# Optimization experiments

Hardware: AMD Instinct MI355X
Metric: run time of the kernel (lower is better)

The kernel has to match this reference:

```python
import jax, jax.numpy as jnp
import numpy as np

N = 50000      # nodes
E = 400000     # edges
HID = 128      # hidden_size
L = 3          # num_att_layer
K = 9          # rbf_size
H = 4          # heads
C = HID // H   # out_channels per head (32)
G = 512        # graphs in batch
CUTOFF = 10.0


def _rbf(D):
    # ExponentialRBF: softplus(softplus_inverse(x)) == x, so centers/widths are the raw values
    centers = jnp.linspace(1.0, float(np.exp(-CUTOFF)), K)          # (K,)
    width = (0.5 / ((1.0 - np.exp(-CUTOFF)) / K)) ** 2              # scalar
    x = D / CUTOFF
    x3 = x ** 3
    x4 = x3 * x
    x5 = x4 * x
    cut = jnp.where(x < 1.0, 1.0 - 6.0 * x5 + 15.0 * x4 - 10.0 * x3, 0.0)
    return cut[:, None] * jnp.exp(-width * (jnp.exp(-D)[:, None] - centers) ** 2)  # (E,K)


def _ln(x, g, b):
    mu = jnp.mean(x, axis=-1, keepdims=True)
    var = jnp.var(x, axis=-1, keepdims=True)
    return (x - mu) / jnp.sqrt(var + 1e-5) * g + b


def _seg_softmax(logits, seg, n):
    # numerically stable softmax over edges grouped by target node
    m = jax.ops.segment_max(logits, seg, num_segments=n)
    e = jnp.exp(logits - m[seg])
    s = jax.ops.segment_sum(e, seg, num_segments=n)
    return e / s[seg]


def setup_inputs() -> dict:
    key = jax.random.key(0)
    ks = jax.random.split(key, 32)
    s = 1.0 / np.sqrt(HID)
    se = 1.0 / np.sqrt(K + 1)
    sb = 1.0 / np.sqrt(3 * HID)
    nrm = jax.random.normal
    inp = {
        "h": nrm(ks[0], (N, HID), jnp.float32),
        "pos": nrm(ks[1], (N, 3), jnp.float32) * 3.0,
        "edge_weight": jax.random.uniform(ks[2], (E,), jnp.float32),
        "Wq": nrm(ks[3], (L, HID, HID)) * s,   "bq": nrm(ks[4], (L, HID)) * 0.01,
        "Wk": nrm(ks[5], (L, HID, HID)) * s,   "bk": nrm(ks[6], (L, HID)) * 0.01,
        "Wv": nrm(ks[7], (L, HID, HID)) * s,   "bv": nrm(ks[8], (L, HID)) * 0.01,
        "We": nrm(ks[9], (L, K + 1, HID)) * se,
        "Wskip": nrm(ks[10], (L, HID, HID)) * s, "bskip": nrm(ks[11], (L, HID)) * 0.01,
        "Wbeta": nrm(ks[12], (L, 3 * HID, 1)) * sb,
        "Wffn1": nrm(ks[13], (L, HID, HID)) * s, "bffn1": nrm(ks[14], (L, HID)) * 0.01,
        "Wffn2": nrm(ks[15], (L, HID, HID)) * s, "bffn2": nrm(ks[16], (L, HID)) * 0.01,
        "Wffn3": nrm(ks[17], (L, HID, HID)) * s, "bffn3": nrm(ks[18], (L, HID)) * 0.01,
        "ln_g": jnp.ones((HID,), jnp.float32),
        "ln_b": jnp.zeros((HID,), jnp.float32),
        "Wo1": nrm(ks[19], (HID, HID)) * s, "bo1": nrm(ks[20], (HID,)) * 0.01,
        "Wo2": nrm(ks[21], (HID, 1)) * s,   "bo2": nrm(ks[22], (1,)) * 0.01,
        "edge_index": jax.random.randint(ks[23], (2, E), 0, N),
        "batch": jnp.sort(jax.random.randint(ks[24], (N,), 0, G)),
    }
    return inp


def reference(h, pos, edge_weight, Wq, bq, Wk, bk, Wv, bv, We, Wskip, bskip, Wbeta,
              Wffn1, bffn1, Wffn2, bffn2, Wffn3, bffn3, ln_g, ln_b, Wo1, bo1, Wo2, bo2,
              edge_index, batch):
    sp = jax.nn.softplus
    n = h.shape[0]
    src, dst = edge_index[0], edge_index[1]  # source j -> target i
    D = jnp.linalg.norm(pos[dst] - pos[src], axis=-1)              # (E,)
    efeat = jnp.concatenate([_rbf(D), edge_weight[:, None]], -1)   # (E, K+1)
    inv_sqrt_c = 1.0 / np.sqrt(C)

    for i in range(L):
        hn = _ln(h, ln_g, ln_b)
        q = (hn @ Wq[i] + bq[i]).reshape(n, H, C)
        k = (hn @ Wk[i] + bk[i]).reshape(n, H, C)
        v = (hn @ Wv[i] + bv[i]).reshape(n, H, C)
        ea = (efeat @ We[i]).reshape(-1, H, C)                     # (E,H,C)
        kj = k[src] + ea
        alpha = jnp.einsum('ehc,ehc->eh', q[dst], kj) * inv_sqrt_c  # (E,H)
        alpha = _seg_softmax(alpha, dst, n)
        # dropout p=0.5 is a no-op in eval mode
        msg = (v[src] + ea) * alpha[:, :, None]
        out = jax.ops.segment_sum(msg, dst, num_segments=n).reshape(n, H * C)
        x_r = hn @ Wskip[i] + bskip[i]
        beta = jax.nn.sigmoid(jnp.concatenate([out, x_r, out - x_r], -1) @ Wbeta[i])
        out = beta * x_r + (1.0 - beta) * out
        h = hn + sp(out)
        hn2 = _ln(h, ln_g, ln_b)
        f = sp(hn2 @ Wffn1[i] + bffn1[i])
        f = sp(f @ Wffn2[i] + bffn2[i])
        f = sp(f @ Wffn3[i] + bffn3[i])
        h = hn2 + f

    pooled = jax.ops.segment_sum(h, batch, num_segments=G)          # (G, HID)
    return sp(pooled @ Wo1 + bo1) @ Wo2 + bo2                       # (G, 1)
```

## Files before the change

### kernel.cpp

```cpp
#include <hip/hip_runtime.h>
#include <hip/hip_bf16.h>
#include <math.h>

#define HID 128
#define KRBF 9
#define NLAYER 3
#define QSSTR 320
#define KVSTR 256
#define QWCOLS 576

typedef __attribute__((ext_vector_type(8))) short bf16x8;
typedef __attribute__((ext_vector_type(4))) float f32x4;

__device__ __forceinline__ float sp_(float x){ return fmaxf(x,0.f) + log1pf(expf(-fabsf(x))); }
__device__ __forceinline__ float sigm_(float x){ return 1.f/(1.f+expf(-x)); }
__device__ __forceinline__ float b2f(short s){
  union{unsigned u; float f;} x; x.u = ((unsigned)(unsigned short)s)<<16; return x.f;
}
__device__ __forceinline__ float wsum64(float v){
  #pragma unroll
  for(int m=1;m<64;m<<=1) v += __shfl_xor(v,m,64);
  return v;
}
__device__ __forceinline__ float wsum16(float v){
  #pragma unroll
  for(int m=1;m<16;m<<=1) v += __shfl_xor(v,m,64);
  return v;
}
__device__ __forceinline__ float2 ldbf2(const __hip_bfloat16* p){
  __hip_bfloat162 b = *(const __hip_bfloat162*)p;
  return make_float2(__bfloat162float(b.x), __bfloat162float(b.y));
}
__device__ __forceinline__ int lb_(const int* __restrict__ a, int n, int key){
  int lo=0, hi=n;
  while(lo<hi){ int mid=(lo+hi)>>1; if(a[mid]<key) lo=mid+1; else hi=mid; }
  return lo;
}

__global__ void count_dst(const int* __restrict__ ei, int* __restrict__ counts, int E){
  int e = blockIdx.x*256+threadIdx.x;
  if(e<E) atomicAdd(&counts[ei[E+e]],1);
}
__global__ void scan1(const int* __restrict__ counts, int* __restrict__ tmp,
                      int* __restrict__ bsums, int N){
  __shared__ int lds[256];
  int t = threadIdx.x; int idx = blockIdx.x*256+t;
  int v = (idx<N)? counts[idx]:0;
  lds[t]=v; __syncthreads();
  for(int off=1;off<256;off<<=1){
    int x = (t>=off)? lds[t-off]:0;
    __syncthreads();
    lds[t]+=x; __syncthreads();
  }
  if(idx<N) tmp[idx]=lds[t];
  if(t==255) bsums[blockIdx.x]=lds[255];
}
__global__ void scan2(const int* __restrict__ bsums, int* __restrict__ boffs, int nb){
  __shared__ int lds[256];
  int t=threadIdx.x;
  int v = (t<nb)? bsums[t]:0;
  lds[t]=v; __syncthreads();
  for(int off=1;off<256;off<<=1){
    int x=(t>=off)?lds[t-off]:0;
    __syncthreads();
    lds[t]+=x; __syncthreads();
  }
  if(t<nb) boffs[t] = lds[t]-v;
}
__global__ void finalize_rs(const int* __restrict__ tmp, const int* __restrict__ boffs,
                            int* __restrict__ row_start, int N){
  int idx = blockIdx.x*256+threadIdx.x;
  if(idx<N) row_start[idx+1] = tmp[idx] + boffs[idx>>8];
  if(idx==0) row_start[0]=0;
}

__global__ void edge_prep(const float* __restrict__ pos, const float* __restrict__ ew,
                          const int* __restrict__ ei, const int* __restrict__ rowst,
                          int* __restrict__ counts2, float* __restrict__ efs,
                          int* __restrict__ esrc, int E){
  int e = blockIdx.x*256 + threadIdx.x;
  if(e>=E) return;
  int s = ei[e], d = ei[E+e];
  float dx = pos[d*3+0]-pos[s*3+0];
  float dy = pos[d*3+1]-pos[s*3+1];
  float dz = pos[d*3+2]-pos[s*3+2];
  float D = sqrtf(dx*dx+dy*dy+dz*dz);
  float x = D*0.1f;
  float cut = 0.f;
  if(x < 1.f){ float x3=x*x*x, x4=x3*x, x5=x4*x; cut = 1.f - 6.f*x5 + 15.f*x4 - 10.f*x3; }
  float ed = expf(-D);
  const double e10 = 4.5399929762484854e-05;
  const float step  = (float)((e10 - 1.0)/8.0);
  const float width = (float)((4.5/(1.0-e10))*(4.5/(1.0-e10)));
  float r12[12];
  #pragma unroll
  for(int k=0;k<KRBF;k++){
    float c = 1.0f + k*step;
    float dd = ed - c;
    r12[k] = cut*expf(-width*dd*dd);
  }
  r12[9] = ew[e]; r12[10]=0.f; r12[11]=0.f;
  int p = rowst[d] + atomicAdd(&counts2[d],1);
  float* o = efs + (size_t)p*12;
  *(float4*)&o[0] = *(float4*)&r12[0];
  *(float4*)&o[4] = *(float4*)&r12[4];
  *(float4*)&o[8] = *(float4*)&r12[8];
  esrc[p] = s;
}

__global__ void pack_w(const float* __restrict__ Wq, const float* __restrict__ Wk,
                       const float* __restrict__ Wv, const float* __restrict__ Wsk,
                       const float* __restrict__ bq, const float* __restrict__ bk,
                       const float* __restrict__ bv, const float* __restrict__ bsk,
                       const float* __restrict__ We,
                       const float* __restrict__ W1, const float* __restrict__ W2,
                       const float* __restrict__ W3,
                       __hip_bfloat16* __restrict__ Wqkvs, float* __restrict__ bqkvs,
                       __hip_bfloat16* __restrict__ Wffn){
  int idx = blockIdx.x*256 + threadIdx.x;
  const int QT = NLAYER*QWCOLS*128;
  const int FT = NLAYER*3*128*128;
  const int BT = NLAYER*QWCOLS;
  if(idx < QT){
    int l = idx / (QWCOLS*128);
    int rem = idx - l*(QWCOLS*128);
    int col = rem >> 7, k = rem & 127;
    float v;
    if(col < 512){
      const float* src = (col<128)?Wq:((col<256)?Wk:((col<384)?Wv:Wsk));
      v = src[(size_t)l*16384 + k*128 + (col&127)];
    } else if(col < 552){
      int j = col-512; int h=j/10; int r=j-10*h;
      const float* wq = Wq + (size_t)l*16384 + k*128;
      const float* we = We + (size_t)l*1280 + r*128;
      float acc=0.f;
      #pragma unroll 8
      for(int c=32*h;c<32*h+32;c++) acc = fmaf(wq[c], we[c], acc);
      v = acc;
    } else v = 0.f;
    Wqkvs[idx] = __float2bfloat16(v);
  } else if(idx < QT+FT){
    int j = idx - QT;
    int k = j & 127; int n = (j>>7)&127; int f = (j>>14)%3; int l = j/(3*16384);
    const float* src = (f==0)?W1:((f==1)?W2:W3);
    Wffn[j] = __float2bfloat16(src[(size_t)l*16384 + k*128 + n]);
  } else if(idx < QT+FT+BT){
    int j = idx - QT - FT;
    int l = j/QWCOLS; int col = j - l*QWCOLS;
    float v;
    if(col<512){
      const float* src = (col<128)?bq:((col<256)?bk:((col<384)?bv:bsk));
      v = src[l*128 + (col&127)];
    } else if(col<552){
      int jj=col-512; int h=jj/10; int r=jj-10*h;
      const float* bqp = bq + l*128;
      const float* we = We + (size_t)l*1280 + r*128;
      float acc=0.f;
      for(int c=32*h;c<32*h+32;c++) acc = fmaf(bqp[c], we[c], acc);
      v = acc;
    } else v = 0.f;
    bqkvs[j] = v;
  }
}

__global__ void ln_node(const float* __restrict__ h, const float* __restrict__ g,
                        const float* __restrict__ b, __hip_bfloat16* __restrict__ hn, int N){
  int n = blockIdx.x*4 + (threadIdx.x>>6);
  if(n>=N) return;
  int lane = threadIdx.x & 63;
  int c = 2*lane;
  float2 v = *(const float2*)&h[(size_t)n*HID + c];
  float s1 = wsum64(v.x+v.y);
  float s2 = wsum64(v.x*v.x+v.y*v.y);
  float mu = s1*(1.f/HID);
  float var = s2*(1.f/HID) - mu*mu;
  float rs = rsqrtf(var + 1e-5f);
  __hip_bfloat162 o;
  o.x = __float2bfloat16((v.x-mu)*rs*g[c]   + b[c]);
  o.y = __float2bfloat16((v.y-mu)*rs*g[c+1] + b[c+1]);
  *(__hip_bfloat162*)&hn[(size_t)n*HID + c] = o;
}

__global__ __launch_bounds__(256) void gemm_mfma(
    const __hip_bfloat16* __restrict__ A, const __hip_bfloat16* __restrict__ Wt,
    const float* __restrict__ bias, const __hip_bfloat16* __restrict__ res,
    void* __restrict__ out0, void* __restrict__ out1,
    const float* __restrict__ lng, const float* __restrict__ lnb,
    int N, int ncols, int mode){
  __shared__ __hip_bfloat16 As[128][136];
  __shared__ __hip_bfloat16 Ws[128][136];
  int row0 = blockIdx.y*128;
  int col0 = blockIdx.x*128;
  int tid = threadIdx.x;
  {
    int chunk = tid&15; int rbase = tid>>4;
    #pragma unroll
    for(int i=0;i<8;i++){
      int r = rbase + 16*i;
      int row = row0 + r;
      float4 v = make_float4(0.f,0.f,0.f,0.f);
      if(row < N) v = *(const float4*)&A[(size_t)row*128 + chunk*8];
      *(float4*)&As[r][chunk*8] = v;
    }
    #pragma unroll
    for(int i=0;i<8;i++){
      int c = rbase + 16*i;
      float4 v = make_float4(0.f,0.f,0.f,0.f);
      if(col0 + c < ncols) v = *(const float4*)&Wt[(size_t)(col0+c)*128 + chunk*8];
      *(float4*)&Ws[c][chunk*8] = v;
    }
  }
  __syncthreads();
  int lane = tid&63;
  int m0 = (tid>>6)*32;
  int ql = lane>>4;
  int il = lane&15;
  f32x4 acc[2][8];
  #pragma unroll
  for(int mi=0;mi<2;mi++)
    #pragma unroll
    for(int nj=0;nj<8;nj++)
      acc[mi][nj] = (f32x4){0.f,0.f,0.f,0.f};
  #pragma unroll
  for(int kk=0;kk<128;kk+=32){
    bf16x8 a0 = *(bf16x8*)&As[m0+il][kk+ql*8];
    bf16x8 a1 = *(bf16x8*)&As[m0+16+il][kk+ql*8];
    bf16x8 bb[8];
    #pragma unroll
    for(int nj=0;nj<8;nj++) bb[nj] = *(bf16x8*)&Ws[nj*16+il][kk+ql*8];
    #pragma unroll
    for(int nj=0;nj<8;nj++){
      acc[0][nj] = __builtin_amdgcn_mfma_f32_16x16x32_bf16(a0, bb[nj], acc[0][nj], 0,0,0);
      acc[1][nj] = __builtin_amdgcn_mfma_f32_16x16x32_bf16(a1, bb[nj], acc[1][nj], 0,0,0);
    }
  }
  if(mode==0){
    __hip_bfloat16* qs  = (__hip_bfloat16*)out0;
    __hip_bfloat16* kvb = (__hip_bfloat16*)out1;
    #pragma unroll
    for(int mi=0;mi<2;mi++){
      int rowb = row0 + m0 + mi*16 + ql*4;
      #pragma unroll
      for(int r=0;r<4;r++){
        int rr = rowb + r;
        if(rr >= N) continue;
        #pragma unroll
        for(int nj=0;nj<8;nj++){
          int cg = col0 + nj*16 + il;
          if(cg >= QWCOLS) continue;
          float t = acc[mi][nj][r] + bias[cg];
          __hip_bfloat16 bv = __float2bfloat16(t);
          if(cg < 128)      qs[(size_t)rr*QSSTR + cg] = bv;
          else if(cg < 384) kvb[(size_t)rr*KVSTR + (cg-128)] = bv;
          else if(cg < 512) qs[(size_t)rr*QSSTR + 128 + (cg-384)] = bv;
          else if(cg < 552) qs[(size_t)rr*QSSTR + 256 + (cg-512)] = bv;
        }
      }
    }
  } else if(mode==1){
    __hip_bfloat16* o = (__hip_bfloat16*)out0;
    #pragma unroll
    for(int mi=0;mi<2;mi++){
      int rowb = row0 + m0 + mi*16 + ql*4;
      #pragma unroll
      for(int r=0;r<4;r++){
        int rr = rowb + r;
        if(rr >= N) continue;
        #pragma unroll
        for(int nj=0;nj<8;nj++){
          int cg = nj*16 + il;
          o[(size_t)rr*128 + cg] = __float2bfloat16(sp_(acc[mi][nj][r] + bias[cg]));
        }
      }
    }
  } else {
    float* hout = (float*)out0;
    __hip_bfloat16* hnout = (__hip_bfloat16*)out1;
    #pragma unroll
    for(int mi=0;mi<2;mi++){
      int rowb = row0 + m0 + mi*16 + ql*4;
      float t[8][4];
      #pragma unroll
      for(int r=0;r<4;r++){
        int rr = rowb + r;
        bool ok = rr < N;
        #pragma unroll
        for(int nj=0;nj<8;nj++){
          int cg = nj*16 + il;
          float x = sp_(acc[mi][nj][r] + bias[cg]);
          float rv = ok ? __bfloat162float(res[(size_t)rr*128 + cg]) : 0.f;
          t[nj][r] = x + rv;
        }
      }
      #pragma unroll
      for(int r=0;r<4;r++){
        int rr = rowb + r;
        if(rr >= N) continue;
        float s1=0.f, s2=0.f;
        #pragma unroll
        for(int nj=0;nj<8;nj++){ float v=t[nj][r]; s1+=v; s2+=v*v; }
        s1 = wsum16(s1); s2 = wsum16(s2);
        float mu = s1*(1.f/128.f);
        float var = s2*(1.f/128.f) - mu*mu;
        float rs = rsqrtf(var + 1e-5f);
        #pragma unroll
        for(int nj=0;nj<8;nj++){
          int cg = nj*16 + il;
          float tv = t[nj][r];
          hout[(size_t)rr*128 + cg] = tv;
          hnout[(size_t)rr*128 + cg] = __float2bfloat16((tv-mu)*rs*lng[cg] + lnb[cg]);
        }
      }
    }
  }
}

__global__ __launch_bounds__(256) void attn_fused2(
    const __hip_bfloat16* __restrict__ qs, const __hip_bfloat16* __restrict__ kvb,
    const float* __restrict__ efs, const int* __restrict__ esrc,
    const float* __restrict__ WeL, const int* __restrict__ rowst,
    float* __restrict__ att, int N){
  int n = blockIdx.x*4 + (threadIdx.x>>6);
  if(n>=N) return;
  int lane = threadIdx.x & 63;
  int eg = lane>>4, sl = lane&15;
  int c8 = sl*8, hd = sl>>2;
  const __hip_bfloat16* rowq = qs + (size_t)n*QSSTR;
  float q8[8];
  {
    bf16x8 qv = *(const bf16x8*)&rowq[c8];
    #pragma unroll
    for(int j=0;j<8;j++) q8[j] = b2f(qv[j]);
  }
  float QW[10];
  #pragma unroll
  for(int r=0;r<10;r++) QW[r] = __bfloat162float(rowq[256 + hd*10 + r]);
  int lo = rowst[n], hi = rowst[n+1];
  float ssum = 0.f;
  float a8[8]; float S[10];
  #pragma unroll
  for(int j=0;j<8;j++) a8[j]=0.f;
  #pragma unroll
  for(int r=0;r<10;r++) S[r]=0.f;
  int i = lo + eg;
  if(i < hi){
    int s = esrc[i];
    const __hip_bfloat16* kr = kvb + (size_t)s*KVSTR;
    bf16x8 kc = *(const bf16x8*)&kr[c8];
    bf16x8 vc = *(const bf16x8*)&kr[128 + c8];
    const float* ef = efs + (size_t)i*12;
    float4 e0 = *(const float4*)&ef[0];
    float4 e1 = *(const float4*)&ef[4];
    float2 e2 = *(const float2*)&ef[8];
    while(true){
      int inext = i + 4;
      bool more = inext < hi;
      bf16x8 kn = kc, vn = vc;
      float4 f0 = e0, f1 = e1; float2 f2 = e2;
      if(more){
        int s2 = esrc[inext];
        const __hip_bfloat16* kr2 = kvb + (size_t)s2*KVSTR;
        kn = *(const bf16x8*)&kr2[c8];
        vn = *(const bf16x8*)&kr2[128 + c8];
        const float* ef2 = efs + (size_t)inext*12;
        f0 = *(const float4*)&ef2[0];
        f1 = *(const float4*)&ef2[4];
        f2 = *(const float2*)&ef2[8];
      }
      float d = 0.f;
      #pragma unroll
      for(int j=0;j<8;j++) d = fmaf(q8[j], b2f(kc[j]), d);
      d += __shfl_xor(d,1,64); d += __shfl_xor(d,2,64);
      float lg = d;
      lg = fmaf(e0.x,QW[0],lg); lg = fmaf(e0.y,QW[1],lg);
      lg = fmaf(e0.z,QW[2],lg); lg = fmaf(e0.w,QW[3],lg);
      lg = fmaf(e1.x,QW[4],lg); lg = fmaf(e1.y,QW[5],lg);
      lg = fmaf(e1.z,QW[6],lg); lg = fmaf(e1.w,QW[7],lg);
      lg = fmaf(e2.x,QW[8],lg); lg = fmaf(e2.y,QW[9],lg);
      lg *= 0.17677669529663687f;
      lg = fminf(lg, 80.f);
      float w = __expf(lg);
      ssum += w;
      #pragma unroll
      for(int j=0;j<8;j++) a8[j] = fmaf(w, b2f(vc[j]), a8[j]);
      S[0]=fmaf(w,e0.x,S[0]); S[1]=fmaf(w,e0.y,S[1]); S[2]=fmaf(w,e0.z,S[2]);
      S[3]=fmaf(w,e0.w,S[3]); S[4]=fmaf(w,e1.x,S[4]); S[5]=fmaf(w,e1.y,S[5]);
      S[6]=fmaf(w,e1.z,S[6]); S[7]=fmaf(w,e1.w,S[7]); S[8]=fmaf(w,e2.x,S[8]);
      S[9]=fmaf(w,e2.y,S[9]);
      if(!more) break;
      kc = kn; vc = vn; e0 = f0; e1 = f1; e2 = f2;
      i = inext;
    }
  }
  #pragma unroll
  for(int m=16;m<64;m<<=1){
    ssum += __shfl_xor(ssum,m,64);
    #pragma unroll
    for(int j=0;j<8;j++) a8[j] += __shfl_xor(a8[j],m,64);
    #pragma unroll
    for(int r=0;r<10;r++) S[r] += __shfl_xor(S[r],m,64);
  }
  float inv = (hi>lo)? 1.f/ssum : 0.f;
  float o8[8];
  #pragma unroll
  for(int j=0;j<8;j++) o8[j]=a8[j];
  #pragma unroll
  for(int r=0;r<10;r++){
    float s=S[r];
    float4 wa = *(const float4*)&WeL[r*128+c8];
    float4 wb = *(const float4*)&WeL[r*128+c8+4];
    o8[0]=fmaf(s,wa.x,o8[0]); o8[1]=fmaf(s,wa.y,o8[1]);
    o8[2]=fmaf(s,wa.z,o8[2]); o8[3]=fmaf(s,wa.w,o8[3]);
    o8[4]=fmaf(s,wb.x,o8[4]); o8[5]=fmaf(s,wb.y,o8[5]);
    o8[6]=fmaf(s,wb.z,o8[6]); o8[7]=fmaf(s,wb.w,o8[7]);
  }
  if(eg==0){
    float4 v0 = make_float4(o8[0]*inv, o8[1]*inv, o8[2]*inv, o8[3]*inv);
    float4 v1 = make_float4(o8[4]*inv, o8[5]*inv, o8[6]*inv, o8[7]*inv);
    *(float4*)&att[(size_t)n*128 + c8]     = v0;
    *(float4*)&att[(size_t)n*128 + c8 + 4] = v1;
  }
}

__global__ void combine_ln(const float* __restrict__ att, const __hip_bfloat16* __restrict__ qs,
                           const __hip_bfloat16* __restrict__ hn, const float* __restrict__ Wb,
                           const float* __restrict__ g, const float* __restrict__ b,
                           __hip_bfloat16* __restrict__ hn2, int N){
  int n = blockIdx.x*4 + (threadIdx.x>>6);
  if(n>=N) return;
  int lane = threadIdx.x&63;
  int c = 2*lane;
  float2 o  = *(const float2*)&att[(size_t)n*HID+c];
  float2 xr = ldbf2(&qs[(size_t)n*QSSTR + 128 + c]);
  float bl = o.x*Wb[c] + o.y*Wb[c+1]
           + xr.x*Wb[HID+c] + xr.y*Wb[HID+c+1]
           + (o.x-xr.x)*Wb[2*HID+c] + (o.y-xr.y)*Wb[2*HID+c+1];
  bl = wsum64(bl);
  float beta = sigm_(bl);
  float u0 = beta*xr.x + (1.f-beta)*o.x;
  float u1 = beta*xr.y + (1.f-beta)*o.y;
  float2 hnv = ldbf2(&hn[(size_t)n*HID+c]);
  float h0 = hnv.x + sp_(u0);
  float h1 = hnv.y + sp_(u1);
  float s1 = wsum64(h0+h1);
  float s2 = wsum64(h0*h0+h1*h1);
  float mu = s1*(1.f/HID);
  float var = s2*(1.f/HID)-mu*mu;
  float rs = rsqrtf(var+1e-5f);
  __hip_bfloat162 outv;
  outv.x = __float2bfloat16((h0-mu)*rs*g[c]+b[c]);
  outv.y = __float2bfloat16((h1-mu)*rs*g[c+1]+b[c+1]);
  *(__hip_bfloat162*)&hn2[(size_t)n*HID+c] = outv;
}

__global__ void pool_head(const float* __restrict__ h, const int* __restrict__ batch,
                          const float* __restrict__ Wo1, const float* __restrict__ bo1,
                          const float* __restrict__ Wo2, const float* __restrict__ bo2,
                          float* __restrict__ out, int N){
  int gid = blockIdx.x;
  int t = threadIdx.x;
  int lo = lb_(batch, N, gid), hi = lb_(batch, N, gid+1);
  __shared__ float pl[128];
  __shared__ float red[128];
  float s = 0.f;
  for(int i=lo;i<hi;i++) s += h[(size_t)i*HID + t];
  pl[t] = s;
  __syncthreads();
  float acc = bo1[t];
  for(int c=0;c<128;c++) acc = fmaf(pl[c], Wo1[c*HID+t], acc);
  red[t] = sp_(acc)*Wo2[t];
  __syncthreads();
  for(int off=64;off>0;off>>=1){
    if(t<off) red[t]+=red[t+off];
    __syncthreads();
  }
  if(t==0) out[gid] = red[0] + bo2[0];
}

extern "C" void kernel_launch(void* const* d_in, const int* in_sizes, int n_in,
                              void* d_out, int out_size, void* d_ws, size_t ws_size,
                              hipStream_t stream){
  const float* h_in = (const float*)d_in[0];
  const float* pos  = (const float*)d_in[1];
  const float* ew   = (const float*)d_in[2];
  const float* Wq = (const float*)d_in[3];  const float* bq = (const float*)d_in[4];
  const float* Wk = (const float*)d_in[5];  const float* bk = (const float*)d_in[6];
  const float* Wv = (const float*)d_in[7];  const float* bv = (const float*)d_in[8];
  const float* We = (const float*)d_in[9];
  const float* Wsk= (const float*)d_in[10]; const float* bsk=(const float*)d_in[11];
  const float* Wbeta=(const float*)d_in[12];
  const float* W1=(const float*)d_in[13]; const float* b1=(const float*)d_in[14];
  const float* W2=(const float*)d_in[15]; const float* b2=(const float*)d_in[16];
  const float* W3=(const float*)d_in[17]; const float* b3=(const float*)d_in[18];
  const float* lng=(const float*)d_in[19]; const float* lnb=(const float*)d_in[20];
  const float* Wo1=(const float*)d_in[21]; const float* bo1=(const float*)d_in[22];
  const float* Wo2=(const float*)d_in[23]; const float* bo2=(const float*)d_in[24];
  const int* ei    = (const int*)d_in[25];
  const int* batch = (const int*)d_in[26];
  int N = in_sizes[0]/HID;
  int E = in_sizes[2];
  int G = out_size;
  float* out = (float*)d_out;

  char* ws = (char*)d_ws;
  size_t off=0;
  auto alloc=[&](size_t bytes)->char*{
    char* p = ws + off;
    off = (off + bytes + 255) & ~(size_t)255;
    return p;
  };
  float* efs   =(float*)alloc((size_t)E*12*4);
  int* esrc    =(int*)  alloc((size_t)E*4);
  int* counts  =(int*)  alloc((size_t)N*4);
  int* counts2 =(int*)  alloc((size_t)N*4);
  int* rowst   =(int*)  alloc((size_t)(N+1)*4);
  int* tmp     =(int*)  alloc((size_t)N*4);
  int* bsums   =(int*)  alloc(256*4);
  int* boffs   =(int*)  alloc(256*4);
  __hip_bfloat16* hn   =(__hip_bfloat16*)alloc((size_t)N*HID*2);
  __hip_bfloat16* hn2  =(__hip_bfloat16*)alloc((size_t)N*HID*2);
  __hip_bfloat16* qsb  =(__hip_bfloat16*)alloc((size_t)N*QSSTR*2);
  __hip_bfloat16* kvb  =(__hip_bfloat16*)alloc((size_t)N*KVSTR*2);
  __hip_bfloat16* f1   =(__hip_bfloat16*)alloc((size_t)N*HID*2);
  __hip_bfloat16* f2   =(__hip_bfloat16*)alloc((size_t)N*HID*2);
  float* att   =(float*)alloc((size_t)N*HID*4);
  float* hcur  =(float*)alloc((size_t)N*HID*4);
  __hip_bfloat16* Wqkvs_t =(__hip_bfloat16*)alloc((size_t)NLAYER*QWCOLS*128*2);
  __hip_bfloat16* Wffn_t  =(__hip_bfloat16*)alloc((size_t)NLAYER*3*128*128*2);
  float* bqkvs =(float*)alloc((size_t)NLAYER*QWCOLS*4);

  int ebl = (E+255)/256;
  int nb  = (N+255)/256;
  int nwb = (N+3)/4;
  int nrb = (N+127)/128;
  dim3 gqkvs((QWCOLS+127)/128, nrb);
  dim3 gffn(1, nrb);

  hipMemsetAsync(counts, 0, (size_t)N*4, stream);
  hipMemsetAsync(counts2,0, (size_t)N*4, stream);
  count_dst<<<ebl,256,0,stream>>>(ei,counts,E);
  scan1<<<nb,256,0,stream>>>(counts,tmp,bsums,N);
  scan2<<<1,256,0,stream>>>(bsums,boffs,nb);
  finalize_rs<<<nb,256,0,stream>>>(tmp,boffs,rowst,N);
  edge_prep<<<ebl,256,0,stream>>>(pos,ew,ei,rowst,counts2,efs,esrc,E);
  {
    int tot = NLAYER*QWCOLS*128 + NLAYER*3*128*128 + NLAYER*QWCOLS;
    pack_w<<<(tot+255)/256,256,0,stream>>>(Wq,Wk,Wv,Wsk,bq,bk,bv,bsk,We,W1,W2,W3,
                                           Wqkvs_t,bqkvs,Wffn_t);
  }

  ln_node<<<nwb,256,0,stream>>>(h_in,lng,lnb,hn,N);
  for(int l=0;l<NLAYER;l++){
    const float* We_l = We + (size_t)l*(KRBF+1)*HID;
    const float* Wb_l = Wbeta + (size_t)l*3*HID;
    const float* b1_l = b1 + (size_t)l*HID;
    const float* b2_l = b2 + (size_t)l*HID;
    const float* b3_l = b3 + (size_t)l*HID;

    gemm_mfma<<<gqkvs,256,0,stream>>>(hn, Wqkvs_t + (size_t)l*QWCOLS*128, bqkvs + l*QWCOLS,
                                      nullptr, qsb, kvb, lng, lnb, N, QWCOLS, 0);
    attn_fused2<<<nwb,256,0,stream>>>(qsb,kvb,efs,esrc,We_l,rowst,att,N);
    combine_ln<<<nwb,256,0,stream>>>(att,qsb,hn,Wb_l,lng,lnb,hn2,N);
    gemm_mfma<<<gffn,256,0,stream>>>(hn2, Wffn_t + (size_t)(l*3+0)*16384, b1_l,
                                     nullptr, f1, nullptr, lng, lnb, N, 128, 1);
    gemm_mfma<<<gffn,256,0,stream>>>(f1,  Wffn_t + (size_t)(l*3+1)*16384, b2_l,
                                     nullptr, f2, nullptr, lng, lnb, N, 128, 1);
    gemm_mfma<<<gffn,256,0,stream>>>(f2,  Wffn_t + (size_t)(l*3+2)*16384, b3_l,
                                     hn2, hcur, hn, lng, lnb, N, 128, 2);
  }
  pool_head<<<G,128,0,stream>>>(hcur,batch,Wo1,bo1,Wo2,bo2,out,N);
}
```

Measured before the change: 1.055 ms.

## Fuse attention with combine/LN, fuse 3-GEMM FFN, permute weights for vector stores

Merges the beta-gating combine and LayerNorm into the attention kernel, dropping the fp32 att buffer round trip. The three FFN GEMMs become one kernel that keeps intermediates in LDS. Weight columns are permuted so GEMM epilogues write 8 contiguous bf16 per lane, and the A operand now goes straight to registers instead of through LDS. Edge CSR construction is split into scatter, per-segment insertion sort and feature kernels so edge order is deterministic, adding two small preprocessing launches and a fp32 side buffer for the q·We projections.

```diff
diff --git a/kernel.cpp b/kernel.cpp
--- a/kernel.cpp
+++ b/kernel.cpp
@@ -5,9 +5,7 @@
 #define HID 128
 #define KRBF 9
 #define NLAYER 3
-#define QSSTR 320
-#define KVSTR 256
-#define QWCOLS 576
+#define QWCOLS 640
 
 typedef __attribute__((ext_vector_type(8))) short bf16x8;
 typedef __attribute__((ext_vector_type(4))) float f32x4;
@@ -17,6 +15,10 @@
 __device__ __forceinline__ float b2f(short s){
   union{unsigned u; float f;} x; x.u = ((unsigned)(unsigned short)s)<<16; return x.f;
 }
+__device__ __forceinline__ short f2bs(float x){
+  __hip_bfloat16 b = __float2bfloat16(x);
+  return *reinterpret_cast<short*>(&b);
+}
 __device__ __forceinline__ float wsum64(float v){
   #pragma unroll
   for(int m=1;m<64;m<<=1) v += __shfl_xor(v,m,64);
@@ -26,10 +28,6 @@
   #pragma unroll
   for(int m=1;m<16;m<<=1) v += __shfl_xor(v,m,64);
   return v;
-}
-__device__ __forceinline__ float2 ldbf2(const __hip_bfloat16* p){
-  __hip_bfloat162 b = *(const __hip_bfloat162*)p;
-  return make_float2(__bfloat162float(b.x), __bfloat162float(b.y));
 }
 __device__ __forceinline__ int lb_(const int* __restrict__ a, int n, int key){
   int lo=0, hi=n;
@@ -73,13 +71,30 @@
   if(idx<N) row_start[idx+1] = tmp[idx] + boffs[idx>>8];
   if(idx==0) row_start[0]=0;
 }
-
-__global__ void edge_prep(const float* __restrict__ pos, const float* __restrict__ ew,
-                          const int* __restrict__ ei, const int* __restrict__ rowst,
-                          int* __restrict__ counts2, float* __restrict__ efs,
-                          int* __restrict__ esrc, int E){
-  int e = blockIdx.x*256 + threadIdx.x;
+__global__ void csr_scatter(const int* __restrict__ ei, const int* __restrict__ rowst,
+                            int* __restrict__ counts2, int* __restrict__ csr, int E){
+  int e = blockIdx.x*256+threadIdx.x;
   if(e>=E) return;
+  int d = ei[E+e];
+  int p = rowst[d] + atomicAdd(&counts2[d],1);
+  csr[p] = e;
+}
+__global__ void sort_seg(const int* __restrict__ rowst, int* __restrict__ csr, int N){
+  int n = blockIdx.x*256+threadIdx.x;
+  if(n>=N) return;
+  int lo=rowst[n], hi=rowst[n+1];
+  for(int i=lo+1;i<hi;i++){
+    int v=csr[i]; int j=i-1;
+    while(j>=lo && csr[j]>v){ csr[j+1]=csr[j]; j--; }
+    csr[j+1]=v;
+  }
+}
+__global__ void edge_feat(const float* __restrict__ pos, const float* __restrict__ ew,
+                          const int* __restrict__ ei, const int* __restrict__ csr,
+                          float* __restrict__ efs, int* __restrict__ esrc, int E){
+  int p = blockIdx.x*256 + threadIdx.x;
+  if(p>=E) return;
+  int e = csr[p];
   int s = ei[e], d = ei[E+e];
   float dx = pos[d*3+0]-pos[s*3+0];
   float dy = pos[d*3+1]-pos[s*3+1];
@@ -100,7 +115,6 @@
     r12[k] = cut*expf(-width*dd*dd);
   }
   r12[9] = ew[e]; r12[10]=0.f; r12[11]=0.f;
-  int p = rowst[d] + atomicAdd(&counts2[d],1);
   float* o = efs + (size_t)p*12;
   *(float4*)&o[0] = *(float4*)&r12[0];
   *(float4*)&o[4] = *(float4*)&r12[4];
@@ -124,30 +138,34 @@
   if(idx < QT){
     int l = idx / (QWCOLS*128);
     int rem = idx - l*(QWCOLS*128);
-    int col = rem >> 7, k = rem & 127;
-    float v;
-    if(col < 512){
-      const float* src = (col<128)?Wq:((col<256)?Wk:((col<384)?Wv:Wsk));
-      v = src[(size_t)l*16384 + k*128 + (col&127)];
-    } else if(col < 552){
-      int j = col-512; int h=j/10; int r=j-10*h;
+    int colp = rem >> 7, k = rem & 127;
+    int b = colp >> 7, p = colp & 127;
+    int g = ((p&15)<<3) + (p>>4);
+    int gcol = b*128 + g;
+    float v = 0.f;
+    if(gcol < 512){
+      const float* src = (gcol<128)?Wq:((gcol<256)?Wk:((gcol<384)?Wv:Wsk));
+      v = src[(size_t)l*16384 + k*128 + (gcol&127)];
+    } else if(gcol < 552){
+      int j = gcol-512; int h=j/10; int r=j-10*h;
       const float* wq = Wq + (size_t)l*16384 + k*128;
       const float* we = We + (size_t)l*1280 + r*128;
       float acc=0.f;
       #pragma unroll 8
       for(int c=32*h;c<32*h+32;c++) acc = fmaf(wq[c], we[c], acc);
       v = acc;
-    } else v = 0.f;
+    }
     Wqkvs[idx] = __float2bfloat16(v);
   } else if(idx < QT+FT){
     int j = idx - QT;
-    int k = j & 127; int n = (j>>7)&127; int f = (j>>14)%3; int l = j/(3*16384);
+    int k = j & 127; int colp = (j>>7)&127; int f = (j>>14)%3; int l = j/(3*16384);
+    int g = ((colp&15)<<3) + (colp>>4);
     const float* src = (f==0)?W1:((f==1)?W2:W3);
-    Wffn[j] = __float2bfloat16(src[(size_t)l*16384 + k*128 + n]);
+    Wffn[j] = __float2bfloat16(src[(size_t)l*16384 + k*128 + g]);
   } else if(idx < QT+FT+BT){
     int j = idx - QT - FT;
     int l = j/QWCOLS; int col = j - l*QWCOLS;
-    float v;
+    float v = 0.f;
     if(col<512){
       const float* src = (col<128)?bq:((col<256)?bk:((col<384)?bv:bsk));
       v = src[l*128 + (col&127)];
@@ -158,7 +176,7 @@
       float acc=0.f;
       for(int c=32*h;c<32*h+32;c++) acc = fmaf(bqp[c], we[c], acc);
       v = acc;
-    } else v = 0.f;
+    }
     bqkvs[j] = v;
   }
 }
@@ -181,163 +199,113 @@
   *(__hip_bfloat162*)&hn[(size_t)n*HID + c] = o;
 }
 
-__global__ __launch_bounds__(256) void gemm_mfma(
+__global__ __launch_bounds__(256) void gemm_qkvs(
     const __hip_bfloat16* __restrict__ A, const __hip_bfloat16* __restrict__ Wt,
-    const float* __restrict__ bias, const __hip_bfloat16* __restrict__ res,
-    void* __restrict__ out0, void* __restrict__ out1,
-    const float* __restrict__ lng, const float* __restrict__ lnb,
-    int N, int ncols, int mode){
-  __shared__ __hip_bfloat16 As[128][136];
-  __shared__ __hip_bfloat16 Ws[128][136];
+    const float* __restrict__ bias,
+    __hip_bfloat16* __restrict__ qsO, __hip_bfloat16* __restrict__ kvO,
+    float* __restrict__ qwO, int N){
+  __shared__ __hip_bfloat16 Ws[128][140];
   int row0 = blockIdx.y*128;
-  int col0 = blockIdx.x*128;
+  int cb = blockIdx.x;
   int tid = threadIdx.x;
   {
-    int chunk = tid&15; int rbase = tid>>4;
+    int chunk = tid&15, rbase = tid>>4;
     #pragma unroll
     for(int i=0;i<8;i++){
-      int r = rbase + 16*i;
-      int row = row0 + r;
-      float4 v = make_float4(0.f,0.f,0.f,0.f);
-      if(row < N) v = *(const float4*)&A[(size_t)row*128 + chunk*8];
-      *(float4*)&As[r][chunk*8] = v;
-    }
-    #pragma unroll
-    for(int i=0;i<8;i++){
-      int c = rbase + 16*i;
-      float4 v = make_float4(0.f,0.f,0.f,0.f);
-      if(col0 + c < ncols) v = *(const float4*)&Wt[(size_t)(col0+c)*128 + chunk*8];
-      *(float4*)&Ws[c][chunk*8] = v;
-    }
-  }
-  __syncthreads();
+      int p = rbase + 16*i;
+      *(float4*)&Ws[p][chunk*8] =
+        *(const float4*)&Wt[(size_t)(cb*128+p)*128 + chunk*8];
+    }
+  }
   int lane = tid&63;
   int m0 = (tid>>6)*32;
-  int ql = lane>>4;
-  int il = lane&15;
+  int ql = lane>>4, il = lane&15;
+  bf16x8 af[2][4];
+  #pragma unroll
+  for(int mi=0;mi<2;mi++){
+    int r = row0 + m0 + mi*16 + il;
+    r = (r < N) ? r : (N-1);
+    const __hip_bfloat16* ap = A + (size_t)r*128 + ql*8;
+    #pragma unroll
+    for(int kc=0;kc<4;kc++) af[mi][kc] = *(const bf16x8*)(ap + kc*32);
+  }
+  __syncthreads();
   f32x4 acc[2][8];
   #pragma unroll
   for(int mi=0;mi<2;mi++)
     #pragma unroll
-    for(int nj=0;nj<8;nj++)
-      acc[mi][nj] = (f32x4){0.f,0.f,0.f,0.f};
-  #pragma unroll
-  for(int kk=0;kk<128;kk+=32){
-    bf16x8 a0 = *(bf16x8*)&As[m0+il][kk+ql*8];
-    bf16x8 a1 = *(bf16x8*)&As[m0+16+il][kk+ql*8];
-    bf16x8 bb[8];
-    #pragma unroll
-    for(int nj=0;nj<8;nj++) bb[nj] = *(bf16x8*)&Ws[nj*16+il][kk+ql*8];
+    for(int nj=0;nj<8;nj++) acc[mi][nj] = (f32x4){0.f,0.f,0.f,0.f};
+  #pragma unroll
+  for(int kc=0;kc<4;kc++){
     #pragma unroll
     for(int nj=0;nj<8;nj++){
-      acc[0][nj] = __builtin_amdgcn_mfma_f32_16x16x32_bf16(a0, bb[nj], acc[0][nj], 0,0,0);
-      acc[1][nj] = __builtin_amdgcn_mfma_f32_16x16x32_bf16(a1, bb[nj], acc[1][nj], 0,0,0);
-    }
-  }
-  if(mode==0){
-    __hip_bfloat16* qs  = (__hip_bfloat16*)out0;
-    __hip_bfloat16* kvb = (__hip_bfloat16*)out1;
-    #pragma unroll
-    for(int mi=0;mi<2;mi++){
-      int rowb = row0 + m0 + mi*16 + ql*4;
+      bf16x8 bb = *(bf16x8*)&Ws[nj*16+il][kc*32+ql*8];
       #pragma unroll
-      for(int r=0;r<4;r++){
-        int rr = rowb + r;
-        if(rr >= N) continue;
+      for(int mi=0;mi<2;mi++)
+        acc[mi][nj] = __builtin_amdgcn_mfma_f32_16x16x32_bf16(af[mi][kc], bb, acc[mi][nj], 0,0,0);
+    }
+  }
+  float bl8[8];
+  {
+    float4 b0 = *(const float4*)&bias[cb*128 + il*8];
+    float4 b1 = *(const float4*)&bias[cb*128 + il*8 + 4];
+    bl8[0]=b0.x; bl8[1]=b0.y; bl8[2]=b0.z; bl8[3]=b0.w;
+    bl8[4]=b1.x; bl8[5]=b1.y; bl8[6]=b1.z; bl8[7]=b1.w;
+  }
+  #pragma unroll
+  for(int mi=0;mi<2;mi++){
+    #pragma unroll
+    for(int r=0;r<4;r++){
+      int rr = row0 + m0 + mi*16 + ql*4 + r;
+      if(rr >= N) continue;
+      if(cb < 4){
+        bf16x8 o;
+        #pragma unroll
+        for(int nj=0;nj<8;nj++) o[nj] = f2bs(acc[mi][nj][r] + bl8[nj]);
+        __hip_bfloat16* dst;
+        if(cb==0)      dst = qsO + (size_t)rr*256 + il*8;
+        else if(cb==1) dst = kvO + (size_t)rr*256 + il*8;
+        else if(cb==2) dst = kvO + (size_t)rr*256 + 128 + il*8;
+        else           dst = qsO + (size_t)rr*256 + 128 + il*8;
+        *(bf16x8*)dst = o;
+      } else if(il < 5){
         #pragma unroll
         for(int nj=0;nj<8;nj++){
-          int cg = col0 + nj*16 + il;
-          if(cg >= QWCOLS) continue;
-          float t = acc[mi][nj][r] + bias[cg];
-          __hip_bfloat16 bv = __float2bfloat16(t);
-          if(cg < 128)      qs[(size_t)rr*QSSTR + cg] = bv;
-          else if(cg < 384) kvb[(size_t)rr*KVSTR + (cg-128)] = bv;
-          else if(cg < 512) qs[(size_t)rr*QSSTR + 128 + (cg-384)] = bv;
-          else if(cg < 552) qs[(size_t)rr*QSSTR + 256 + (cg-512)] = bv;
+          int g = il*8 + nj;
+          int h = g/10, rb = g - 10*h;
+          qwO[(size_t)rr*48 + h*12 + rb] = acc[mi][nj][r] + bl8[nj];
         }
       }
     }
-  } else if(mode==1){
-    __hip_bfloat16* o = (__hip_bfloat16*)out0;
-    #pragma unroll
-    for(int mi=0;mi<2;mi++){
-      int rowb = row0 + m0 + mi*16 + ql*4;
-      #pragma unroll
-      for(int r=0;r<4;r++){
-        int rr = rowb + r;
-        if(rr >= N) continue;
-        #pragma unroll
-        for(int nj=0;nj<8;nj++){
-          int cg = nj*16 + il;
-          o[(size_t)rr*128 + cg] = __float2bfloat16(sp_(acc[mi][nj][r] + bias[cg]));
-        }
-      }
-    }
-  } else {
-    float* hout = (float*)out0;
-    __hip_bfloat16* hnout = (__hip_bfloat16*)out1;
-    #pragma unroll
-    for(int mi=0;mi<2;mi++){
-      int rowb = row0 + m0 + mi*16 + ql*4;
-      float t[8][4];
-      #pragma unroll
-      for(int r=0;r<4;r++){
-        int rr = rowb + r;
-        bool ok = rr < N;
-        #pragma unroll
-        for(int nj=0;nj<8;nj++){
-          int cg = nj*16 + il;
-          float x = sp_(acc[mi][nj][r] + bias[cg]);
-          float rv = ok ? __bfloat162float(res[(size_t)rr*128 + cg]) : 0.f;
-          t[nj][r] = x + rv;
-        }
-      }
-      #pragma unroll
-      for(int r=0;r<4;r++){
-        int rr = rowb + r;
-        if(rr >= N) continue;
-        float s1=0.f, s2=0.f;
-        #pragma unroll
-        for(int nj=0;nj<8;nj++){ float v=t[nj][r]; s1+=v; s2+=v*v; }
-        s1 = wsum16(s1); s2 = wsum16(s2);
-        float mu = s1*(1.f/128.f);
-        float var = s2*(1.f/128.f) - mu*mu;
-        float rs = rsqrtf(var + 1e-5f);
-        #pragma unroll
-        for(int nj=0;nj<8;nj++){
-          int cg = nj*16 + il;
-          float tv = t[nj][r];
-          hout[(size_t)rr*128 + cg] = tv;
-          hnout[(size_t)rr*128 + cg] = __float2bfloat16((tv-mu)*rs*lng[cg] + lnb[cg]);
-        }
-      }
-    }
-  }
-}
-
-__global__ __launch_bounds__(256) void attn_fused2(
+  }
+}
+
+__global__ __launch_bounds__(256) void attn_fused4(
     const __hip_bfloat16* __restrict__ qs, const __hip_bfloat16* __restrict__ kvb,
-    const float* __restrict__ efs, const int* __restrict__ esrc,
-    const float* __restrict__ WeL, const int* __restrict__ rowst,
-    float* __restrict__ att, int N){
+    const float* __restrict__ qwb, const float* __restrict__ efs,
+    const int* __restrict__ esrc, const float* __restrict__ WeL,
+    const int* __restrict__ rowst, const __hip_bfloat16* __restrict__ hn,
+    const float* __restrict__ Wb, const float* __restrict__ lng,
+    const float* __restrict__ lnb, __hip_bfloat16* __restrict__ hn2, int N){
   int n = blockIdx.x*4 + (threadIdx.x>>6);
   if(n>=N) return;
   int lane = threadIdx.x & 63;
   int eg = lane>>4, sl = lane&15;
   int c8 = sl*8, hd = sl>>2;
-  const __hip_bfloat16* rowq = qs + (size_t)n*QSSTR;
+  const __hip_bfloat16* rowq = qs + (size_t)n*256;
   float q8[8];
   {
     bf16x8 qv = *(const bf16x8*)&rowq[c8];
     #pragma unroll
     for(int j=0;j<8;j++) q8[j] = b2f(qv[j]);
   }
-  float QW[10];
-  #pragma unroll
-  for(int r=0;r<10;r++) QW[r] = __bfloat162float(rowq[256 + hd*10 + r]);
+  const float* qwp = qwb + (size_t)n*48 + hd*12;
+  float4 qa = *(const float4*)qwp;
+  float4 qb = *(const float4*)(qwp+4);
+  float2 qc = *(const float2*)(qwp+8);
+  float QW[10] = {qa.x,qa.y,qa.z,qa.w,qb.x,qb.y,qb.z,qb.w,qc.x,qc.y};
   int lo = rowst[n], hi = rowst[n+1];
-  float ssum = 0.f;
-  float a8[8]; float S[10];
+  float ssum = 0.f, a8[8], S[10];
   #pragma unroll
   for(int j=0;j<8;j++) a8[j]=0.f;
   #pragma unroll
@@ -345,7 +313,7 @@
   int i = lo + eg;
   if(i < hi){
     int s = esrc[i];
-    const __hip_bfloat16* kr = kvb + (size_t)s*KVSTR;
+    const __hip_bfloat16* kr = kvb + (size_t)s*256;
     bf16x8 kc = *(const bf16x8*)&kr[c8];
     bf16x8 vc = *(const bf16x8*)&kr[128 + c8];
     const float* ef = efs + (size_t)i*12;
@@ -359,7 +327,7 @@
       float4 f0 = e0, f1 = e1; float2 f2 = e2;
       if(more){
         int s2 = esrc[inext];
-        const __hip_bfloat16* kr2 = kvb + (size_t)s2*KVSTR;
+        const __hip_bfloat16* kr2 = kvb + (size_t)s2*256;
         kn = *(const bf16x8*)&kr2[c8];
         vn = *(const bf16x8*)&kr2[128 + c8];
         const float* ef2 = efs + (size_t)inext*12;
@@ -414,43 +382,179 @@
     o8[4]=fmaf(s,wb.x,o8[4]); o8[5]=fmaf(s,wb.y,o8[5]);
     o8[6]=fmaf(s,wb.z,o8[6]); o8[7]=fmaf(s,wb.w,o8[7]);
   }
+  #pragma unroll
+  for(int j=0;j<8;j++) o8[j] *= inv;
+  float xr8[8];
+  {
+    bf16x8 xv = *(const bf16x8*)&rowq[128 + c8];
+    #pragma unroll
+    for(int j=0;j<8;j++) xr8[j] = b2f(xv[j]);
+  }
+  float wb0[8], wb1[8], wb2[8];
+  {
+    float4 a0=*(const float4*)&Wb[c8],     a1=*(const float4*)&Wb[c8+4];
+    float4 b0=*(const float4*)&Wb[128+c8], b1=*(const float4*)&Wb[128+c8+4];
+    float4 c0=*(const float4*)&Wb[256+c8], c1=*(const float4*)&Wb[256+c8+4];
+    wb0[0]=a0.x;wb0[1]=a0.y;wb0[2]=a0.z;wb0[3]=a0.w;wb0[4]=a1.x;wb0[5]=a1.y;wb0[6]=a1.z;wb0[7]=a1.w;
+    wb1[0]=b0.x;wb1[1]=b0.y;wb1[2]=b0.z;wb1[3]=b0.w;wb1[4]=b1.x;wb1[5]=b1.y;wb1[6]=b1.z;wb1[7]=b1.w;
+    wb2[0]=c0.x;wb2[1]=c0.y;wb2[2]=c0.z;wb2[3]=c0.w;wb2[4]=c1.x;wb2[5]=c1.y;wb2[6]=c1.z;wb2[7]=c1.w;
+  }
+  float pb = 0.f;
+  #pragma unroll
+  for(int j=0;j<8;j++)
+    pb += o8[j]*wb0[j] + xr8[j]*wb1[j] + (o8[j]-xr8[j])*wb2[j];
+  pb = wsum16(pb);
+  float beta = sigm_(pb);
+  float h8[8], s1=0.f, s2=0.f;
+  {
+    bf16x8 hv = *(const bf16x8*)&hn[(size_t)n*128 + c8];
+    #pragma unroll
+    for(int j=0;j<8;j++){
+      float u = beta*xr8[j] + (1.f-beta)*o8[j];
+      float x = b2f(hv[j]) + sp_(u);
+      h8[j]=x; s1+=x; s2+=x*x;
+    }
+  }
+  s1 = wsum16(s1); s2 = wsum16(s2);
+  float mu = s1*(1.f/128.f);
+  float var = s2*(1.f/128.f) - mu*mu;
+  float rsg = rsqrtf(var + 1e-5f);
   if(eg==0){
-    float4 v0 = make_float4(o8[0]*inv, o8[1]*inv, o8[2]*inv, o8[3]*inv);
-    float4 v1 = make_float4(o8[4]*inv, o8[5]*inv, o8[6]*inv, o8[7]*inv);
-    *(float4*)&att[(size_t)n*128 + c8]     = v0;
-    *(float4*)&att[(size_t)n*128 + c8 + 4] = v1;
-  }
-}
-
-__global__ void combine_ln(const float* __restrict__ att, const __hip_bfloat16* __restrict__ qs,
-                           const __hip_bfloat16* __restrict__ hn, const float* __restrict__ Wb,
-                           const float* __restrict__ g, const float* __restrict__ b,
-                           __hip_bfloat16* __restrict__ hn2, int N){
-  int n = blockIdx.x*4 + (threadIdx.x>>6);
-  if(n>=N) return;
-  int lane = threadIdx.x&63;
-  int c = 2*lane;
-  float2 o  = *(const float2*)&att[(size_t)n*HID+c];
-  float2 xr = ldbf2(&qs[(size_t)n*QSSTR + 128 + c]);
-  float bl = o.x*Wb[c] + o.y*Wb[c+1]
-           + xr.x*Wb[HID+c] + xr.y*Wb[HID+c+1]
-           + (o.x-xr.x)*Wb[2*HID+c] + (o.y-xr.y)*Wb[2*HID+c+1];
-  bl = wsum64(bl);
-  float beta = sigm_(bl);
-  float u0 = beta*xr.x + (1.f-beta)*o.x;
-  float u1 = beta*xr.y + (1.f-beta)*o.y;
-  float2 hnv = ldbf2(&hn[(size_t)n*HID+c]);
-  float h0 = hnv.x + sp_(u0);
-  float h1 = hnv.y + sp_(u1);
-  float s1 = wsum64(h0+h1);
-  float s2 = wsum64(h0*h0+h1*h1);
-  float mu = s1*(1.f/HID);
-  float var = s2*(1.f/HID)-mu*mu;
-  float rs = rsqrtf(var+1e-5f);
-  __hip_bfloat162 outv;
-  outv.x = __float2bfloat16((h0-mu)*rs*g[c]+b[c]);
-  outv.y = __float2bfloat16((h1-mu)*rs*g[c+1]+b[c+1]);
-  *(__hip_bfloat162*)&hn2[(size_t)n*HID+c] = outv;
+    float4 g0=*(const float4*)&lng[c8], g1=*(const float4*)&lng[c8+4];
+    float4 bb0=*(const float4*)&lnb[c8], bb1=*(const float4*)&lnb[c8+4];
+    float g8[8]={g0.x,g0.y,g0.z,g0.w,g1.x,g1.y,g1.z,g1.w};
+    float lb8[8]={bb0.x,bb0.y,bb0.z,bb0.w,bb1.x,bb1.y,bb1.z,bb1.w};
+    bf16x8 o;
+    #pragma unroll
+    for(int j=0;j<8;j++) o[j] = f2bs((h8[j]-mu)*rsg*g8[j] + lb8[j]);
+    *(bf16x8*)&hn2[(size_t)n*128 + c8] = o;
+  }
+}
+
+__global__ __launch_bounds__(256) void ffn_fused(
+    const __hip_bfloat16* __restrict__ hn2, const __hip_bfloat16* __restrict__ Wf,
+    const float* __restrict__ b1, const float* __restrict__ b2,
+    const float* __restrict__ b3, const float* __restrict__ lng,
+    const float* __restrict__ lnb, float* __restrict__ hout,
+    __hip_bfloat16* __restrict__ hnout, int N){
+  __shared__ __hip_bfloat16 Ws[128][140];
+  __shared__ __hip_bfloat16 inter[2][64][140];
+  int row0 = blockIdx.x*64;
+  int tid = threadIdx.x, lane = tid&63, wv = tid>>6;
+  int ql = lane>>4, il = lane&15;
+  int chunk = tid&15, rbase = tid>>4;
+
+  auto stage = [&](const __hip_bfloat16* Wp){
+    #pragma unroll
+    for(int i=0;i<8;i++){
+      int p = rbase + 16*i;
+      *(float4*)&Ws[p][chunk*8] = *(const float4*)&Wp[(size_t)p*128 + chunk*8];
+    }
+  };
+  auto loadbias = [&](const float* bp, float* bl8){
+    float4 x0 = *(const float4*)&bp[il*8];
+    float4 x1 = *(const float4*)&bp[il*8+4];
+    bl8[0]=x0.x; bl8[1]=x0.y; bl8[2]=x0.z; bl8[3]=x0.w;
+    bl8[4]=x1.x; bl8[5]=x1.y; bl8[6]=x1.z; bl8[7]=x1.w;
+  };
+
+  f32x4 acc[8];
+  bf16x8 af[4];
+  stage(Wf);
+  {
+    int r = row0 + wv*16 + il;
+    r = (r<N)? r : (N-1);
+    const __hip_bfloat16* ap = hn2 + (size_t)r*128 + ql*8;
+    #pragma unroll
+    for(int kc=0;kc<4;kc++) af[kc] = *(const bf16x8*)(ap + kc*32);
+  }
+  __syncthreads();
+  #pragma unroll
+  for(int nj=0;nj<8;nj++) acc[nj] = (f32x4){0.f,0.f,0.f,0.f};
+  #pragma unroll
+  for(int kc=0;kc<4;kc++)
+    #pragma unroll
+    for(int nj=0;nj<8;nj++){
+      bf16x8 bb = *(bf16x8*)&Ws[nj*16+il][kc*32+ql*8];
+      acc[nj] = __builtin_amdgcn_mfma_f32_16x16x32_bf16(af[kc], bb, acc[nj], 0,0,0);
+    }
+  {
+    float bl8[8]; loadbias(b1, bl8);
+    #pragma unroll
+    for(int r=0;r<4;r++){
+      int lr = wv*16 + ql*4 + r;
+      bf16x8 o;
+      #pragma unroll
+      for(int nj=0;nj<8;nj++) o[nj] = f2bs(sp_(acc[nj][r] + bl8[nj]));
+      *(bf16x8*)&inter[0][lr][il*8] = o;
+    }
+  }
+  __syncthreads();
+  stage(Wf + 16384);
+  #pragma unroll
+  for(int kc=0;kc<4;kc++) af[kc] = *(bf16x8*)&inter[0][wv*16+il][ql*8 + kc*32];
+  __syncthreads();
+  #pragma unroll
+  for(int nj=0;nj<8;nj++) acc[nj] = (f32x4){0.f,0.f,0.f,0.f};
+  #pragma unroll
+  for(int kc=0;kc<4;kc++)
+    #pragma unroll
+    for(int nj=0;nj<8;nj++){
+      bf16x8 bb = *(bf16x8*)&Ws[nj*16+il][kc*32+ql*8];
+      acc[nj] = __builtin_amdgcn_mfma_f32_16x16x32_bf16(af[kc], bb, acc[nj], 0,0,0);
+    }
+  {
+    float bl8[8]; loadbias(b2, bl8);
+    #pragma unroll
+    for(int r=0;r<4;r++){
+      int lr = wv*16 + ql*4 + r;
+      bf16x8 o;
+      #pragma unroll
+      for(int nj=0;nj<8;nj++) o[nj] = f2bs(sp_(acc[nj][r] + bl8[nj]));
+      *(bf16x8*)&inter[1][lr][il*8] = o;
+    }
+  }
+  __syncthreads();
+  stage(Wf + 2*16384);
+  #pragma unroll
+  for(int kc=0;kc<4;kc++) af[kc] = *(bf16x8*)&inter[1][wv*16+il][ql*8 + kc*32];
+  __syncthreads();
+  #pragma unroll
+  for(int nj=0;nj<8;nj++) acc[nj] = (f32x4){0.f,0.f,0.f,0.f};
+  #pragma unroll
+  for(int kc=0;kc<4;kc++)
+    #pragma unroll
+    for(int nj=0;nj<8;nj++){
+      bf16x8 bb = *(bf16x8*)&Ws[nj*16+il][kc*32+ql*8];
+      acc[nj] = __builtin_amdgcn_mfma_f32_16x16x32_bf16(af[kc], bb, acc[nj], 0,0,0);
+    }
+  {
+    float bl8[8]; loadbias(b3, bl8);
+    float lg8[8], lb8[8];
+    loadbias(lng, lg8); loadbias(lnb, lb8);
+    #pragma unroll
+    for(int r=0;r<4;r++){
+      int rr = row0 + wv*16 + ql*4 + r;
+      if(rr >= N) continue;
+      bf16x8 rv = *(const bf16x8*)&hn2[(size_t)rr*128 + il*8];
+      float t8[8], s1=0.f, s2=0.f;
+      #pragma unroll
+      for(int nj=0;nj<8;nj++){
+        float x = sp_(acc[nj][r] + bl8[nj]) + b2f(rv[nj]);
+        t8[nj]=x; s1+=x; s2+=x*x;
+      }
+      s1 = wsum16(s1); s2 = wsum16(s2);
+      float mu = s1*(1.f/128.f);
+      float var = s2*(1.f/128.f) - mu*mu;
+      float rsg = rsqrtf(var + 1e-5f);
+      *(float4*)&hout[(size_t)rr*128 + il*8]     = make_float4(t8[0],t8[1],t8[2],t8[3]);
+      *(float4*)&hout[(size_t)rr*128 + il*8 + 4] = make_float4(t8[4],t8[5],t8[6],t8[7]);
+      bf16x8 o;
+      #pragma unroll
+      for(int nj=0;nj<8;nj++) o[nj] = f2bs((t8[nj]-mu)*rsg*lg8[nj] + lb8[nj]);
+      *(bf16x8*)&hnout[(size_t)rr*128 + il*8] = o;
+    }
+  }
 }
 
 __global__ void pool_head(const float* __restrict__ h, const int* __restrict__ batch,
@@ -511,6 +615,7 @@
   };
   float* efs   =(float*)alloc((size_t)E*12*4);
   int* esrc    =(int*)  alloc((size_t)E*4);
+  int* csr     =(int*)  alloc((size_t)E*4);
   int* counts  =(int*)  alloc((size_t)N*4);
   int* counts2 =(int*)  alloc((size_t)N*4);
   int* rowst   =(int*)  alloc((size_t)(N+1)*4);
@@ -519,11 +624,9 @@
   int* boffs   =(int*)  alloc(256*4);
   __hip_bfloat16* hn   =(__hip_bfloat16*)alloc((size_t)N*HID*2);
   __hip_bfloat16* hn2  =(__hip_bfloat16*)alloc((size_t)N*HID*2);
-  __hip_bfloat16* qsb  =(__hip_bfloat16*)alloc((size_t)N*QSSTR*2);
-  __hip_bfloat16* kvb  =(__hip_bfloat16*)alloc((size_t)N*KVSTR*2);
-  __hip_bfloat16* f1   =(__hip_bfloat16*)alloc((size_t)N*HID*2);
-  __hip_bfloat16* f2   =(__hip_bfloat16*)alloc((size_t)N*HID*2);
-  float* att   =(float*)alloc((size_t)N*HID*4);
+  __hip_bfloat16* qsb  =(__hip_bfloat16*)alloc((size_t)N*256*2);
+  __hip_bfloat16* kvb  =(__hip_bfloat16*)alloc((size_t)N*256*2);
+  float* qwb   =(float*)alloc((size_t)N*48*4);
   float* hcur  =(float*)alloc((size_t)N*HID*4);
   __hip_bfloat16* Wqkvs_t =(__hip_bfloat16*)alloc((size_t)NLAYER*QWCOLS*128*2);
   __hip_bfloat16* Wffn_t  =(__hip_bfloat16*)alloc((size_t)NLAYER*3*128*128*2);
@@ -532,9 +635,9 @@
   int ebl = (E+255)/256;
   int nb  = (N+255)/256;
   int nwb = (N+3)/4;
-  int nrb = (N+127)/128;
-  dim3 gqkvs((QWCOLS+127)/128, nrb);
-  dim3 gffn(1, nrb);
+  int nrb128 = (N+127)/128;
+  int nrb64  = (N+63)/64;
+  dim3 gqkvs(QWCOLS/128, nrb128);
 
   hipMemsetAsync(counts, 0, (size_t)N*4, stream);
   hipMemsetAsync(counts2,0, (size_t)N*4, stream);
@@ -542,7 +645,9 @@
   scan1<<<nb,256,0,stream>>>(counts,tmp,bsums,N);
   scan2<<<1,256,0,stream>>>(bsums,boffs,nb);
   finalize_rs<<<nb,256,0,stream>>>(tmp,boffs,rowst,N);
-  edge_prep<<<ebl,256,0,stream>>>(pos,ew,ei,rowst,counts2,efs,esrc,E);
+  csr_scatter<<<ebl,256,0,stream>>>(ei,rowst,counts2,csr,E);
+  sort_seg<<<nb,256,0,stream>>>(rowst,csr,N);
+  edge_feat<<<ebl,256,0,stream>>>(pos,ew,ei,csr,efs,esrc,E);
   {
     int tot = NLAYER*QWCOLS*128 + NLAYER*3*128*128 + NLAYER*QWCOLS;
     pack_w<<<(tot+255)/256,256,0,stream>>>(Wq,Wk,Wv,Wsk,bq,bk,bv,bsk,We,W1,W2,W3,
@@ -557,16 +662,12 @@
     const float* b2_l = b2 + (size_t)l*HID;
     const float* b3_l = b3 + (size_t)l*HID;
 
-    gemm_mfma<<<gqkvs,256,0,stream>>>(hn, Wqkvs_t + (size_t)l*QWCOLS*128, bqkvs + l*QWCOLS,
-                                      nullptr, qsb, kvb, lng, lnb, N, QWCOLS, 0);
-    attn_fused2<<<nwb,256,0,stream>>>(qsb,kvb,efs,esrc,We_l,rowst,att,N);
-    combine_ln<<<nwb,256,0,stream>>>(att,qsb,hn,Wb_l,lng,lnb,hn2,N);
-    gemm_mfma<<<gffn,256,0,stream>>>(hn2, Wffn_t + (size_t)(l*3+0)*16384, b1_l,
-                                     nullptr, f1, nullptr, lng, lnb, N, 128, 1);
-    gemm_mfma<<<gffn,256,0,stream>>>(f1,  Wffn_t + (size_t)(l*3+1)*16384, b2_l,
-                                     nullptr, f2, nullptr, lng, lnb, N, 128, 1);
-    gemm_mfma<<<gffn,256,0,stream>>>(f2,  Wffn_t + (size_t)(l*3+2)*16384, b3_l,
-                                     hn2, hcur, hn, lng, lnb, N, 128, 2);
+    gemm_qkvs<<<gqkvs,256,0,stream>>>(hn, Wqkvs_t + (size_t)l*QWCOLS*128,
+                                      bqkvs + l*QWCOLS, qsb, kvb, qwb, N);
+    attn_fused4<<<nwb,256,0,stream>>>(qsb,kvb,qwb,efs,esrc,We_l,rowst,hn,
+                                      Wb_l,lng,lnb,hn2,N);
+    ffn_fused<<<nrb64,256,0,stream>>>(hn2, Wffn_t + (size_t)l*3*16384,
+                                      b1_l,b2_l,b3_l,lng,lnb,hcur,hn,N);
   }
   pool_head<<<G,128,0,stream>>>(hcur,batch,Wo1,bo1,Wo2,bo2,out,N);
 }
```

After: 966.6 us. -8.4%, faster.
